# Kernel tuning notes

Measured on AMD Instinct MI355X. Metric: run time of the kernel, lower is better.

## Reference

```python
import jax, jax.numpy as jnp
import numpy as np

# --- config (mirrors the torch/keras module's config object) ---
RATIOS = np.array([0.5, 1.0, 2.0], dtype=np.float32)
SCALE = 128.0
POS_THRESH = 0.15
NMS_THRESH = 0.7
STRIDE = 16.0
H = W = 64
A = len(RATIOS)           # anchors per spatial location
N = H * W * A             # total anchors = 12288


def _conv(x, w, b):
    # NHWC input, HWIO kernel, SAME padding, stride 1
    y = jax.lax.conv_general_dilated(x, w, (1, 1), 'SAME',
                                     dimension_numbers=('NHWC', 'HWIO', 'NHWC'))
    return y + b


def _grid_anchors():
    ws = SCALE * np.sqrt(RATIOS)
    hs = SCALE / np.sqrt(RATIOS)
    base = np.stack([-ws / 2, -hs / 2, ws / 2, hs / 2], axis=1)      # [A,4]
    xs = (np.arange(W, dtype=np.float32) + 0.5) * STRIDE
    ys = (np.arange(H, dtype=np.float32) + 0.5) * STRIDE
    cx, cy = np.meshgrid(xs, ys)                                     # [H,W]
    shifts = np.stack([cx, cy, cx, cy], axis=-1).reshape(-1, 1, 4)   # [H*W,1,4]
    return jnp.asarray((shifts + base[None]).reshape(-1, 4).astype(np.float32))  # [N,4]


def _decode(anchors, deltas):
    # standard RPN box decode: (dx,dy,dw,dh) applied to (x1,y1,x2,y2) anchors
    w = anchors[:, 2] - anchors[:, 0]
    h = anchors[:, 3] - anchors[:, 1]
    xc = (anchors[:, 0] + anchors[:, 2]) * 0.5 + deltas[:, 0] * w
    yc = (anchors[:, 1] + anchors[:, 3]) * 0.5 + deltas[:, 1] * h
    nw = w * jnp.exp(deltas[:, 2])
    nh = h * jnp.exp(deltas[:, 3])
    return jnp.stack([xc - nw / 2, yc - nh / 2, xc + nw / 2, yc + nh / 2], axis=1)  # [N,4]


def _nms(boxes, keep0, thresh):
    # greedy NMS in index order (original passes scores=ones to tf NMS, so
    # the sort by score is a no-op and greedy order == index order).
    boxes = jax.lax.stop_gradient(boxes)
    x1, y1, x2, y2 = boxes[:, 0], boxes[:, 1], boxes[:, 2], boxes[:, 3]
    areas = (x2 - x1) * (y2 - y1)
    idx = jnp.arange(boxes.shape[0])

    def body(i, keep):
        xx1 = jnp.maximum(x1[i], x1)
        yy1 = jnp.maximum(y1[i], y1)
        xx2 = jnp.minimum(x2[i], x2)
        yy2 = jnp.minimum(y2[i], y2)
        inter = jnp.maximum(xx2 - xx1, 0.0) * jnp.maximum(yy2 - yy1, 0.0)
        iou = inter / (areas[i] + areas - inter + 1e-9)
        suppress = keep[i] & keep & (iou > thresh) & (idx > i)
        return keep & ~suppress

    return jax.lax.fori_loop(0, boxes.shape[0], body, keep0)


def setup_inputs() -> dict:
    key = jax.random.key(0)
    ks = jax.random.split(key, 7)
    c_in, c_mid = 1024, 512
    inputs = jax.random.normal(ks[0], (1, H, W, c_in), dtype=jnp.float32)
    conv_w = jax.random.normal(ks[1], (3, 3, c_in, c_mid), dtype=jnp.float32) * 0.01
    conv_b = jnp.zeros((c_mid,), dtype=jnp.float32)
    cls_w = jax.random.normal(ks[2], (1, 1, c_mid, 2 * A), dtype=jnp.float32) * 0.05
    cls_b = jnp.zeros((2 * A,), dtype=jnp.float32)
    reg_w = jax.random.normal(ks[3], (1, 1, c_mid, 4 * A), dtype=jnp.float32) * 0.01
    reg_b = jnp.zeros((4 * A,), dtype=jnp.float32)
    return {"inputs": inputs, "conv_w": conv_w, "conv_b": conv_b,
            "cls_w": cls_w, "cls_b": cls_b, "reg_w": reg_w, "reg_b": reg_b}


def reference(inputs, conv_w, conv_b, cls_w, cls_b, reg_w, reg_b):
    x = jax.nn.relu(_conv(inputs, conv_w, conv_b))                  # [1,H,W,512]
    cls = jax.nn.softmax(_conv(x, cls_w, cls_b), axis=-1)           # [1,H,W,2A]
    reg = _conv(x, reg_w, reg_b)                                    # [1,H,W,4A]
    scores = cls.reshape(-1, 2)[:, 1]                               # [N] fg prob
    deltas = reg.reshape(-1, 4)                                     # [N,4]
    boxes = _decode(_grid_anchors(), deltas)                        # [N,4]
    keep0 = scores > POS_THRESH
    keep = _nms(boxes, keep0, NMS_THRESH)                           # [N] bool
    # fixed-shape proposal output: suppressed / filtered boxes zeroed out
    return boxes * keep[:, None].astype(boxes.dtype)
```

## Files before the change

### kernel.cpp

```cpp
#include <hip/hip_runtime.h>
#include <cstdint>

#define NBOX 12288
#define NWORDS 192
#define POS_THRESH 0.15f
#define NMS_THRESH 0.7f

typedef unsigned long long u64;
typedef _Float16 half8 __attribute__((ext_vector_type(8)));
typedef float floatx4 __attribute__((ext_vector_type(4)));

__global__ __launch_bounds__(256) void zero_y(float4* __restrict__ Y) {
  Y[blockIdx.x * 256 + threadIdx.x] = float4{0.f, 0.f, 0.f, 0.f};
}

__global__ __launch_bounds__(256) void prep_wt(
    const float* __restrict__ Wc, _Float16* __restrict__ WTh, _Float16* __restrict__ WTl)
{
  __shared__ float tile[64][65];
  const int b = blockIdx.x;
  const int tap = b >> 7;
  const int rem = b & 127;
  const int c0 = (rem >> 3) * 64, n0 = (rem & 7) * 64;
  const int t = threadIdx.x;
  #pragma unroll
  for (int i = 0; i < 16; ++i) {
    const int idx = i * 256 + t;
    const int c = idx >> 6, n = idx & 63;
    tile[n][c] = Wc[((size_t)(tap * 1024 + c0 + c)) * 512 + n0 + n];
  }
  __syncthreads();
  #pragma unroll
  for (int i = 0; i < 16; ++i) {
    const int idx = i * 256 + t;
    const int n = idx >> 6, c = idx & 63;
    const float v = tile[n][c];
    const _Float16 h = (_Float16)v;
    const _Float16 l = (_Float16)((v - (float)h) * 4096.0f);
    const size_t o = ((size_t)(tap * 512 + n0 + n)) * 1024 + c0 + c;
    WTh[o] = h;
    WTl[o] = l;
  }
}

#define AROW 40
#define AS_PLANE (4 * 66 * AROW)
#define BS_PLANE (128 * AROW)
#define YPLANE 2097152
__global__ __launch_bounds__(256, 2) void conv_mfma(
    const float* __restrict__ X, const _Float16* __restrict__ WTh,
    const _Float16* __restrict__ WTl, float* __restrict__ Y, int partial)
{
  __shared__ _Float16 As[2 * AS_PLANE];
  __shared__ _Float16 Bs[2 * BS_PLANE];
  const int bid = blockIdx.x;
  const int ks = bid & 3;
  const int nt = (bid >> 2) & 3;
  const int mt = bid >> 4;
  const int t = threadIdx.x;
  const int lane = t & 63, wid = t >> 6;
  const int wm = wid >> 1, wn = wid & 1;
  const int lrow = lane & 15, quad = lane >> 4;

  floatx4 accH[4][4], accL[4][4];
  #pragma unroll
  for (int i = 0; i < 4; ++i)
    #pragma unroll
    for (int j = 0; j < 4; ++j) { accH[i][j] = (floatx4)0.f; accL[i][j] = (floatx4)0.f; }

  for (int kc = 0; kc < 8; ++kc) {
    const int c0 = ks * 256 + kc * 32;
    __syncthreads();
    for (int r = t; r < 264; r += 256) {
      const int yy = r / 66;
      const int xx = r - yy * 66;
      const int yi = mt * 2 + yy - 1;
      const int xi = xx - 1;
      const int akey = (r >> 3) & 3;
      _Float16* dsth = &As[r * AROW];
      _Float16* dstl = dsth + AS_PLANE;
      if (yi >= 0 && yi < 64 && xi >= 0 && xi < 64) {
        const float4* src = (const float4*)(X + ((size_t)(yi * 64 + xi)) * 1024 + c0);
        #pragma unroll
        for (int j = 0; j < 4; ++j) {
          const float4 va = src[2 * j], vb = src[2 * j + 1];
          const float f[8] = {va.x, va.y, va.z, va.w, vb.x, vb.y, vb.z, vb.w};
          half8 hh, hl;
          #pragma unroll
          for (int e = 0; e < 8; ++e) {
            const _Float16 h = (_Float16)f[e];
            hh[e] = h;
            hl[e] = (_Float16)((f[e] - (float)h) * 4096.0f);
          }
          const int sl = (j ^ akey) * 8;
          *(half8*)&dsth[sl] = hh;
          *(half8*)&dstl[sl] = hl;
        }
      } else {
        const half8 z = (half8)(_Float16)0.f;
        #pragma unroll
        for (int j = 0; j < 4; ++j) { *(half8*)&dsth[j * 8] = z; *(half8*)&dstl[j * 8] = z; }
      }
    }
    for (int tap = 0; tap < 9; ++tap) {
      if (tap > 0) __syncthreads();
      {
        const int hl = t >> 7, n = t & 127;
        const int bkey = (n >> 3) & 3;
        const _Float16* src = (hl ? WTl : WTh) +
            ((size_t)(tap * 512 + nt * 128 + n)) * 1024 + c0;
        _Float16* dst = &Bs[hl * BS_PLANE + n * AROW];
        #pragma unroll
        for (int j = 0; j < 4; ++j)
          *(half8*)&dst[(j ^ bkey) * 8] = *(const half8*)&src[j * 8];
      }
      __syncthreads();
      const int dy = tap / 3 - 1, dx = tap - (tap / 3) * 3 - 1;
      const int yy = wm + dy + 1;
      const int xxb = dx + 1;
      half8 Ah[4], Al[4], Bh[4], Bl[4];
      #pragma unroll
      for (int fm = 0; fm < 4; ++fm) {
        const int row = yy * 66 + xxb + fm * 16 + lrow;
        const int idx = row * AROW + ((quad ^ ((row >> 3) & 3)) * 8);
        Ah[fm] = *(const half8*)&As[idx];
        Al[fm] = *(const half8*)&As[idx + AS_PLANE];
      }
      #pragma unroll
      for (int fn = 0; fn < 4; ++fn) {
        const int row = wn * 64 + fn * 16 + lrow;
        const int idx = row * AROW + ((quad ^ ((row >> 3) & 3)) * 8);
        Bh[fn] = *(const half8*)&Bs[idx];
        Bl[fn] = *(const half8*)&Bs[idx + BS_PLANE];
      }
      #pragma unroll
      for (int fm = 0; fm < 4; ++fm)
        #pragma unroll
        for (int fn = 0; fn < 4; ++fn) {
          accH[fm][fn] = __builtin_amdgcn_mfma_f32_16x16x32_f16(Ah[fm], Bh[fn], accH[fm][fn], 0, 0, 0);
          accL[fm][fn] = __builtin_amdgcn_mfma_f32_16x16x32_f16(Al[fm], Bh[fn], accL[fm][fn], 0, 0, 0);
          accL[fm][fn] = __builtin_amdgcn_mfma_f32_16x16x32_f16(Ah[fm], Bl[fn], accL[fm][fn], 0, 0, 0);
        }
    }
  }
  const int m0 = mt * 128 + wm * 64;
  const int n0 = nt * 128 + wn * 64;
  if (partial) {
    float* Yp = Y + (size_t)ks * YPLANE;
    #pragma unroll
    for (int fm = 0; fm < 4; ++fm)
      #pragma unroll
      for (int fn = 0; fn < 4; ++fn) {
        const int n = n0 + fn * 16 + lrow;
        #pragma unroll
        for (int r = 0; r < 4; ++r) {
          const int m = m0 + fm * 16 + quad * 4 + r;
          Yp[(size_t)m * 512 + n] = accH[fm][fn][r] + accL[fm][fn][r] * (1.0f / 4096.0f);
        }
      }
  } else {
    #pragma unroll
    for (int fm = 0; fm < 4; ++fm)
      #pragma unroll
      for (int fn = 0; fn < 4; ++fn) {
        const int n = n0 + fn * 16 + lrow;
        #pragma unroll
        for (int r = 0; r < 4; ++r) {
          const int m = m0 + fm * 16 + quad * 4 + r;
          atomicAdd(&Y[(size_t)m * 512 + n],
                    accH[fm][fn][r] + accL[fm][fn][r] * (1.0f / 4096.0f));
        }
      }
  }
}

__global__ __launch_bounds__(64) void heads_decode(
    const float* __restrict__ Yx, int nparts, const float* __restrict__ Bc,
    const float* __restrict__ Wcls, const float* __restrict__ bcls,
    const float* __restrict__ Wreg, const float* __restrict__ breg,
    float* __restrict__ boxes, float* __restrict__ scores, int* __restrict__ ext)
{
  __shared__ float xs[512];
  const int pos = blockIdx.x;
  const int l = threadIdx.x;
  if (l == 0 && pos < NWORDS) ext[pos] = pos;
  float4 v0 = {0.f, 0.f, 0.f, 0.f};
  float4 v1 = {0.f, 0.f, 0.f, 0.f};
  for (int p = 0; p < nparts; ++p) {
    const float* xrow = Yx + (size_t)p * YPLANE + (size_t)pos * 512;
    const float4 a = *(const float4*)&xrow[l * 8];
    const float4 b = *(const float4*)&xrow[l * 8 + 4];
    v0.x += a.x; v0.y += a.y; v0.z += a.z; v0.w += a.w;
    v1.x += b.x; v1.y += b.y; v1.z += b.z; v1.w += b.w;
  }
  const float4 b0 = *(const float4*)&Bc[l * 8];
  const float4 b1 = *(const float4*)&Bc[l * 8 + 4];
  xs[l * 8 + 0] = fmaxf(v0.x + b0.x, 0.f);
  xs[l * 8 + 1] = fmaxf(v0.y + b0.y, 0.f);
  xs[l * 8 + 2] = fmaxf(v0.z + b0.z, 0.f);
  xs[l * 8 + 3] = fmaxf(v0.w + b0.w, 0.f);
  xs[l * 8 + 4] = fmaxf(v1.x + b1.x, 0.f);
  xs[l * 8 + 5] = fmaxf(v1.y + b1.y, 0.f);
  xs[l * 8 + 6] = fmaxf(v1.z + b1.z, 0.f);
  xs[l * 8 + 7] = fmaxf(v1.w + b1.w, 0.f);
  __syncthreads();

  const float* wp;
  int oc;
  float bini;
  if (l < 6)       { wp = Wcls + l;       oc = 6;  bini = bcls[l]; }
  else if (l < 18) { wp = Wreg + (l - 6); oc = 12; bini = breg[l - 6]; }
  else             { wp = Wcls;           oc = 0;  bini = 0.f; }
  float acc = bini;
  const float* p = wp;
  #pragma unroll 4
  for (int c = 0; c < 512; ++c) { acc = fmaf(xs[c], *p, acc); p += oc; }

  const float l0 = __shfl(acc, 0), l1 = __shfl(acc, 1), l2 = __shfl(acc, 2);
  const float l3 = __shfl(acc, 3), l4 = __shfl(acc, 4), l5 = __shfl(acc, 5);
  const int a = (l < 3) ? l : 0;
  const float d0 = __shfl(acc, 6 + a * 4 + 0);
  const float d1 = __shfl(acc, 6 + a * 4 + 1);
  const float d2 = __shfl(acc, 6 + a * 4 + 2);
  const float d3 = __shfl(acc, 6 + a * 4 + 3);

  const float mx = fmaxf(fmaxf(fmaxf(l0, l1), fmaxf(l2, l3)), fmaxf(l4, l5));
  const float e0 = expf(l0 - mx), e1 = expf(l1 - mx), e2 = expf(l2 - mx);
  const float e3 = expf(l3 - mx), e4 = expf(l4 - mx), e5 = expf(l5 - mx);
  const float den = ((((e0 + e1) + e2) + e3) + e4) + e5;
  const float esel = (a == 0) ? e1 : ((a == 1) ? e3 : e5);
  const float sc = esel / den;

  const int px = pos & 63, py = pos >> 6;
  const float cx = (px + 0.5f) * 16.0f;
  const float cy = (py + 0.5f) * 16.0f;
  const float ratio = (a == 0) ? 0.5f : ((a == 1) ? 1.0f : 2.0f);
  const float sq = sqrtf(ratio);
  const float wsz = 128.0f * sq;
  const float hsz = 128.0f / sq;
  const float a0 = cx - wsz * 0.5f;
  const float a1 = cy - hsz * 0.5f;
  const float a2 = cx + wsz * 0.5f;
  const float a3 = cy + hsz * 0.5f;
  const float w = a2 - a0, h = a3 - a1;
  const float xc = __fadd_rn(__fmul_rn(__fadd_rn(a0, a2), 0.5f), __fmul_rn(d0, w));
  const float yc = __fadd_rn(__fmul_rn(__fadd_rn(a1, a3), 0.5f), __fmul_rn(d1, h));
  const float nw = __fmul_rn(w, expf(d2));
  const float nh = __fmul_rn(h, expf(d3));
  float4 box;
  box.x = __fsub_rn(xc, __fmul_rn(nw, 0.5f));
  box.y = __fsub_rn(yc, __fmul_rn(nh, 0.5f));
  box.z = __fadd_rn(xc, __fmul_rn(nw, 0.5f));
  box.w = __fadd_rn(yc, __fmul_rn(nh, 0.5f));

  if (l < 3) {
    const int idx = pos * 3 + a;
    *(float4*)&boxes[idx * 4] = box;
    scores[idx] = sc;
  }
}

__global__ __launch_bounds__(256) void build_mask(
    const float* __restrict__ boxes, u64* __restrict__ maskT,
    int* __restrict__ ext)
{
  const int w  = blockIdx.x;
  const int ci = blockIdx.y;
  if (w < ci) return;
  __shared__ float4 rb[64];
  __shared__ int anyf;
  const int t = threadIdx.x;
  const int lane = t & 63, wid = t >> 6;
  if (t == 0) anyf = 0;
  if (t < 64) rb[t] = *(const float4*)&boxes[(ci * 64 + t) * 4];
  const float4 cb = *(const float4*)&boxes[(w * 64 + lane) * 4];
  const float careaa = __fmul_rn(cb.z - cb.x, cb.w - cb.y);
  const int jglob = w * 64 + lane;
  __syncthreads();
  bool any = false;
  for (int rr = 0; rr < 16; ++rr) {
    const int r = wid * 16 + rr;
    const int row = ci * 64 + r;
    const float4 rx = rb[r];
    const float ra = __fmul_rn(rx.z - rx.x, rx.w - rx.y);
    const float xx1 = fmaxf(rx.x, cb.x);
    const float yy1 = fmaxf(rx.y, cb.y);
    const float xx2 = fminf(rx.z, cb.z);
    const float yy2 = fminf(rx.w, cb.w);
    const float iw = fmaxf(__fsub_rn(xx2, xx1), 0.f);
    const float ih = fmaxf(__fsub_rn(yy2, yy1), 0.f);
    const float inter = __fmul_rn(iw, ih);
    const float den = __fadd_rn(__fsub_rn(__fadd_rn(ra, careaa), inter), 1e-9f);
    const float iou = __fdiv_rn(inter, den);
    const bool bit = (iou > NMS_THRESH) && (jglob > row);
    any |= bit;
    const u64 word = __ballot(bit ? 1 : 0);
    if (lane == 0) maskT[(size_t)w * NBOX + row] = word;
  }
  if (any) anyf = 1;
  __syncthreads();
  if (t == 0 && anyf && w > ci) atomicMax(&ext[ci], w);
}

__device__ __forceinline__ u64 rl64(unsigned lo, unsigned hi, int l) {
  const unsigned a = (unsigned)__builtin_amdgcn_readlane((int)lo, l);
  const unsigned b = (unsigned)__builtin_amdgcn_readlane((int)hi, l);
  return ((u64)b << 32) | (u64)a;
}
__device__ __forceinline__ u64 rl64v(u64 v, int ln) {
  const unsigned a = (unsigned)__builtin_amdgcn_readlane((int)(unsigned)v, ln);
  const unsigned b = (unsigned)__builtin_amdgcn_readlane((int)(unsigned)(v >> 32), ln);
  return ((u64)b << 32) | (u64)a;
}
__device__ __forceinline__ u64 shflxor64(u64 v, int m) {
  const int lo = __shfl_xor((int)(unsigned)v, m);
  const int hi = __shfl_xor((int)(unsigned)(v >> 32), m);
  return ((u64)(unsigned)hi << 32) | (unsigned)lo;
}
__device__ __forceinline__ u64 build_alive(const float* sp) {
  u64 w = 0ull;
  const float4* p = (const float4*)sp;
  #pragma unroll
  for (int q = 0; q < 16; ++q) {
    const float4 s = p[q];
    if (s.x > POS_THRESH) w |= (1ull << (q * 4 + 0));
    if (s.y > POS_THRESH) w |= (1ull << (q * 4 + 1));
    if (s.z > POS_THRESH) w |= (1ull << (q * 4 + 2));
    if (s.w > POS_THRESH) w |= (1ull << (q * 4 + 3));
  }
  return w;
}

#define NSTEPF(C_, MU, DU, MP, DP)                                              \
  do {                                                                          \
    if (t < 256) {                                                              \
      const int c_ = (C_);                                                      \
      const int e_ = extS[c_];                                                  \
      const u64 aw0v_ = alvS[c_];                                               \
      if (c_ + 1 < NWORDS) {                                                    \
        DP = maskT[(size_t)(c_ + 1) * NBOX + (size_t)(c_ + 1) * 64 + lane];     \
        const int en_ = extS[c_ + 1];                                           \
        const int t0n_ = c_ + 2 + wsub;                                         \
        if (t0n_ <= en_) {                                                      \
          const u64* cbp_ = maskT + (size_t)t0n_ * NBOX + (size_t)(c_ + 1) * 64 + sub * 8; \
          MP##0 = cbp_[0]; MP##1 = cbp_[1]; MP##2 = cbp_[2]; MP##3 = cbp_[3];   \
          MP##4 = cbp_[4]; MP##5 = cbp_[5]; MP##6 = cbp_[6]; MP##7 = cbp_[7];   \
        }                                                                       \
      }                                                                         \
      const unsigned awlo_ = (unsigned)__builtin_amdgcn_readfirstlane((int)(unsigned)(aw0v_ & 0xffffffffull)); \
      const unsigned awhi_ = (unsigned)__builtin_amdgcn_readfirstlane((int)(unsigned)(aw0v_ >> 32)); \
      const u64 aw0_ = ((u64)awhi_ << 32) | (u64)awlo_;                         \
      if (aw0_) {                                                               \
        const unsigned dlo_ = (unsigned)(DU & 0xffffffffull);                   \
        const unsigned dhi_ = (unsigned)(DU >> 32);                             \
        u64 aw_ = aw0_;                                                         \
        const bool sb_ = ((aw0_ >> lane) & 1ull) && ((DU & aw0_) != 0ull);      \
        u64 pending_ = __ballot(sb_ ? 1 : 0);                                   \
        while (pending_) {                                                      \
          const u64 p0_ = pending_;                                             \
          const u64 p1_ = p0_ & (p0_ - 1);                                      \
          const u64 p2_ = p1_ & (p1_ - 1);                                      \
          const u64 p3_ = p2_ & (p2_ - 1);                                      \
          const int b0_ = __builtin_ctzll(p0_);                                 \
          const int b1_ = p1_ ? __builtin_ctzll(p1_) : 64;                      \
          const int b2_ = p2_ ? __builtin_ctzll(p2_) : 64;                      \
          const int b3_ = p3_ ? __builtin_ctzll(p3_) : 64;                      \
          const u64 r0_ = rl64(dlo_, dhi_, b0_);                                \
          const u64 r1_ = rl64(dlo_, dhi_, b1_ & 63);                           \
          const u64 r2_ = rl64(dlo_, dhi_, b2_ & 63);                           \
          const u64 r3_ = rl64(dlo_, dhi_, b3_ & 63);                           \
          u64 supp_ = r0_;                                                      \
          u64 done_ = 1ull << b0_;                                              \
          const u64 k1_ = ((b1_ < 64) & !((supp_ >> (b1_ & 63)) & 1ull)) ? ~0ull : 0ull; \
          supp_ |= r1_ & k1_;  done_ |= (1ull << (b1_ & 63)) & k1_;             \
          const u64 k2_ = ((b2_ < 64) & !((supp_ >> (b2_ & 63)) & 1ull)) ? ~0ull : 0ull; \
          supp_ |= r2_ & k2_;  done_ |= (1ull << (b2_ & 63)) & k2_;             \
          const u64 k3_ = ((b3_ < 64) & !((supp_ >> (b3_ & 63)) & 1ull)) ? ~0ull : 0ull; \
          supp_ |= r3_ & k3_;  done_ |= (1ull << (b3_ & 63)) & k3_;             \
          aw_ &= ~supp_;                                                        \
          pending_ &= ~(supp_ | done_);                                         \
        }                                                                       \
        const int t0_ = c_ + 1 + wsub;                                          \
        if (t0_ <= e_) {                                                        \
          const unsigned oct_ = (unsigned)(aw_ >> (sub * 8)) & 0xffu;           \
          u64 sup_ = 0ull;                                                      \
          if (oct_ & 1u)   sup_ |= MU##0;                                       \
          if (oct_ & 2u)   sup_ |= MU##1;                                       \
          if (oct_ & 4u)   sup_ |= MU##2;                                       \
          if (oct_ & 8u)   sup_ |= MU##3;                                       \
          if (oct_ & 16u)  sup_ |= MU##4;                                       \
          if (oct_ & 32u)  sup_ |= MU##5;                                       \
          if (oct_ & 64u)  sup_ |= MU##6;                                       \
          if (oct_ & 128u) sup_ |= MU##7;                                       \
          if (sup_) atomicAnd((unsigned long long*)&alvS[t0_], ~sup_);          \
        }                                                                       \
        for (int base_ = c_ + 33; base_ <= e_; base_ += 32) {                   \
          const int tw_ = base_ + wsub;                                         \
          if (tw_ <= e_) {                                                      \
            const u64* cbp_ = maskT + (size_t)tw_ * NBOX + (size_t)c_ * 64 + sub * 8; \
            u64 m_[8];                                                          \
            _Pragma("unroll")                                                   \
            for (int j_ = 0; j_ < 8; ++j_) m_[j_] = cbp_[j_];                   \
            const unsigned oct_ = (unsigned)(aw_ >> (sub * 8)) & 0xffu;         \
            u64 sup_ = 0ull;                                                    \
            _Pragma("unroll")                                                   \
            for (int j_ = 0; j_ < 8; ++j_) if ((oct_ >> j_) & 1u) sup_ |= m_[j_]; \
            if (sup_) atomicAnd((unsigned long long*)&alvS[tw_], ~sup_);        \
          }                                                                     \
        }                                                                       \
        if (t == 0) alvS[c_] = aw_;                                             \
      }                                                                         \
    }                                                                           \
    asm volatile("s_waitcnt lgkmcnt(0)" ::: "memory");                          \
    __builtin_amdgcn_s_barrier();                                               \
    asm volatile("" ::: "memory");                                              \
  } while (0)

__global__ __launch_bounds__(1024) void nms_scan(
    const float* __restrict__ scores, const u64* __restrict__ maskT,
    const int* __restrict__ ext, u64* __restrict__ aliveOut)
{
  __shared__ u64 alvA[NWORDS], alvB[NWORDS], keep0S[NWORDS];
  __shared__ int extS[NWORDS], srcLoS[NWORDS];
  __shared__ int changedS;
  const int t = threadIdx.x;
  const int lane = t & 63;
  const int wv = t >> 6;
  const int g = lane >> 3;
  const int s = lane & 7;
  const int wsub = t >> 3;
  const int sub = t & 7;

  if (t < NWORDS) {
    const u64 wb = build_alive(scores + (size_t)t * 64);
    keep0S[t] = wb;
    alvA[t] = wb;
    extS[t] = ext[t];
  }
  if (t == 0) changedS = 0;
  __syncthreads();
  if (t < NWORDS) {
    int lo = t;
    for (int c = 0; c < t; ++c) if (extS[c] >= t) { lo = c; break; }
    srcLoS[t] = lo;
  }
  __syncthreads();

  int cur = 0, converged = 0;
  for (int it = 0; it < 64; ++it) {
    const u64* aOld = cur ? alvB : alvA;
    u64* aNew = cur ? alvA : alvB;
    for (int k = 0; k < 12; ++k) {
      const int w = wv + k * 16;
      const u64 dg = maskT[(size_t)w * NBOX + (size_t)w * 64 + lane];
      const int lo = srcLoS[w];
      u64 supx = 0ull;
      for (int base = lo; base < w; base += 8) {
        const int c = base + g;
        u64 part = 0ull;
        if (c < w) {
          const u64 av = aOld[c];
          const unsigned oct = (unsigned)((av >> (s * 8)) & 0xffull);
          const u64* col = maskT + (size_t)w * NBOX + (size_t)c * 64 + s * 8;
          const u64 m0 = col[0], m1 = col[1], m2 = col[2], m3 = col[3];
          const u64 m4 = col[4], m5 = col[5], m6 = col[6], m7 = col[7];
          if (oct & 1u)   part |= m0;
          if (oct & 2u)   part |= m1;
          if (oct & 4u)   part |= m2;
          if (oct & 8u)   part |= m3;
          if (oct & 16u)  part |= m4;
          if (oct & 32u)  part |= m5;
          if (oct & 64u)  part |= m6;
          if (oct & 128u) part |= m7;
        }
        part |= shflxor64(part, 1);
        part |= shflxor64(part, 2);
        part |= shflxor64(part, 4);
        part |= shflxor64(part, 8);
        part |= shflxor64(part, 16);
        part |= shflxor64(part, 32);
        supx |= part;
      }
      const u64 b0v = keep0S[w] & ~supx;
      u64 aw = b0v;
      const bool sbv = ((b0v >> lane) & 1ull) && ((dg & b0v) != 0ull);
      u64 pending = __ballot(sbv ? 1 : 0);
      while (pending) {
        const u64 q0 = pending;
        const u64 q1 = q0 & (q0 - 1);
        const u64 q2 = q1 & (q1 - 1);
        const u64 q3 = q2 & (q2 - 1);
        const int c0 = __builtin_ctzll(q0);
        const int c1 = q1 ? __builtin_ctzll(q1) : 64;
        const int c2 = q2 ? __builtin_ctzll(q2) : 64;
        const int c3 = q3 ? __builtin_ctzll(q3) : 64;
        const u64 u0 = rl64v(dg, c0);
        const u64 u1 = rl64v(dg, c1 & 63);
        const u64 u2 = rl64v(dg, c2 & 63);
        const u64 u3 = rl64v(dg, c3 & 63);
        u64 sp = u0;
        u64 dn = 1ull << c0;
        const u64 g1 = ((c1 < 64) && !((sp >> (c1 & 63)) & 1ull)) ? ~0ull : 0ull;
        sp |= u1 & g1; dn |= (1ull << (c1 & 63)) & g1;
        const u64 g2 = ((c2 < 64) && !((sp >> (c2 & 63)) & 1ull)) ? ~0ull : 0ull;
        sp |= u2 & g2; dn |= (1ull << (c2 & 63)) & g2;
        const u64 g3 = ((c3 < 64) && !((sp >> (c3 & 63)) & 1ull)) ? ~0ull : 0ull;
        sp |= u3 & g3; dn |= (1ull << (c3 & 63)) & g3;
        aw &= ~sp;
        pending &= ~(sp | dn);
      }
      if (lane == 0) {
        aNew[w] = aw;
        if (aw != aOld[w]) changedS = 1;
      }
    }
    __syncthreads();
    const int ch = changedS;
    __syncthreads();
    cur ^= 1;
    if (!ch) { converged = 1; break; }
    if (t == 0) changedS = 0;
    __syncthreads();
  }

  if (converged) {
    const u64* fin = cur ? alvB : alvA;
    if (t < NWORDS) aliveOut[t] = fin[t];
    return;
  }

  u64* alvS = alvA;
  if (t < NWORDS) alvS[t] = keep0S[t];
  __syncthreads();

  u64 mA0 = 0, mA1 = 0, mA2 = 0, mA3 = 0, mA4 = 0, mA5 = 0, mA6 = 0, mA7 = 0;
  u64 mB0 = 0, mB1 = 0, mB2 = 0, mB3 = 0, mB4 = 0, mB5 = 0, mB6 = 0, mB7 = 0;
  u64 dgA = 0, dgB = 0;
  if (t < 256) {
    const int e0f = extS[0];
    if (1 + wsub <= e0f) {
      const u64* cbp = maskT + (size_t)(1 + wsub) * NBOX + sub * 8;
      mA0 = cbp[0]; mA1 = cbp[1]; mA2 = cbp[2]; mA3 = cbp[3];
      mA4 = cbp[4]; mA5 = cbp[5]; mA6 = cbp[6]; mA7 = cbp[7];
    }
    dgA = maskT[lane];
  }
  asm volatile("s_waitcnt lgkmcnt(0)" ::: "memory");
  __builtin_amdgcn_s_barrier();
  asm volatile("" ::: "memory");

  for (int c = 0; c < NWORDS; c += 2) {
    NSTEPF(c,     mA, dgA, mB, dgB);
    NSTEPF(c + 1, mB, dgB, mA, dgA);
  }
  if (t < NWORDS) aliveOut[t] = alvS[t];
}

__global__ __launch_bounds__(256) void write_output(
    const float* __restrict__ boxes, const u64* __restrict__ alive,
    float* __restrict__ out)
{
  const int i = blockIdx.x * 256 + threadIdx.x;
  if (i < NBOX) {
    const bool k = (alive[i >> 6] >> (i & 63)) & 1ull;
    const float4 b = *(const float4*)&boxes[i * 4];
    const float4 z = {0.f, 0.f, 0.f, 0.f};
    *(float4*)&out[i * 4] = k ? b : z;
  }
}

extern "C" void kernel_launch(void* const* d_in, const int* in_sizes, int n_in,
                              void* d_out, int out_size, void* d_ws, size_t ws_size,
                              hipStream_t stream) {
  const float* X    = (const float*)d_in[0];
  const float* Wc   = (const float*)d_in[1];
  const float* Bc   = (const float*)d_in[2];
  const float* Wcls = (const float*)d_in[3];
  const float* bcls = (const float*)d_in[4];
  const float* Wreg = (const float*)d_in[5];
  const float* breg = (const float*)d_in[6];

  char* ws = (char*)d_ws;
  const size_t NEED_BIG = 52676864ull;

  if (ws_size >= NEED_BIG) {
    float*     Y4     = (float*)    (ws);
    float*     boxes  = (float*)    (ws + 33554432);
    float*     scores = (float*)    (ws + 33751040);
    u64*       aliveG = (u64*)      (ws + 33800192);
    int*       extG   = (int*)      (ws + 33801728);
    _Float16*  WTh    = (_Float16*) (ws + 33802496);
    _Float16*  WTl    = (_Float16*) (ws + 43239680);
    u64*       maskT  = (u64*)      (ws + 33802496);

    prep_wt     <<<1152, 256, 0, stream>>>(Wc, WTh, WTl);
    conv_mfma   <<<512, 256, 0, stream>>>(X, WTh, WTl, Y4, 1);
    heads_decode<<<4096, 64, 0, stream>>>(Y4, 4, Bc, Wcls, bcls, Wreg, breg, boxes, scores, extG);
    build_mask  <<<dim3(192, 192), 256, 0, stream>>>(boxes, maskT, extG);
    nms_scan    <<<1, 1024, 0, stream>>>(scores, maskT, extG, aliveG);
    write_output<<<48, 256, 0, stream>>>(boxes, aliveG, (float*)d_out);
  } else {
    float*     Y      = (float*)    (ws);
    float*     boxes  = (float*)    (ws + 8388608);
    float*     scores = (float*)    (ws + 8585216);
    u64*       aliveG = (u64*)      (ws + 8634368);
    int*       extG   = (int*)      (ws + 8635904);
    _Float16*  WTh    = (_Float16*) (ws + 8636672);
    _Float16*  WTl    = (_Float16*) (ws + 18073856);
    u64*       maskT  = (u64*)      (ws + 8636672);

    zero_y      <<<2048, 256, 0, stream>>>((float4*)Y);
    prep_wt     <<<1152, 256, 0, stream>>>(Wc, WTh, WTl);
    conv_mfma   <<<512, 256, 0, stream>>>(X, WTh, WTl, Y, 0);
    heads_decode<<<4096, 64, 0, stream>>>(Y, 1, Bc, Wcls, bcls, Wreg, breg, boxes, scores, extG);
    build_mask  <<<dim3(192, 192), 256, 0, stream>>>(boxes, maskT, extG);
    nms_scan    <<<1, 1024, 0, stream>>>(scores, maskT, extG, aliveG);
    write_output<<<48, 256, 0, stream>>>(boxes, aliveG, (float*)d_out);
  }
}
```

Before: 490.5 us.

## Use in-place Gauss-Seidel NMS iteration with contiguous word ownership and cached diagonals

The Jacobi-style fixed-point NMS iteration with double-buffered alive bitmasks becomes an in-place Gauss-Seidel update on a single shared array. Each wave now owns a contiguous block of 12 words and processes them in order, so later words immediately see suppression updates from earlier ones, which should cut the number of outer iterations needed to converge. The diagonal mask blocks are preloaded into registers once instead of being re-read every iteration. This adds register pressure and relies on monotonic convergence of in-place updates; the contiguous ownership may also unbalance work across waves.

Measured after the change: 436.5 us, median of 2. -11.0%, faster.

```diff
diff --git a/kernel.cpp b/kernel.cpp
--- a/kernel.cpp
+++ b/kernel.cpp
@@ -420,7 +420,7 @@
     const float* __restrict__ scores, const u64* __restrict__ maskT,
     const int* __restrict__ ext, u64* __restrict__ aliveOut)
 {
-  __shared__ u64 alvA[NWORDS], alvB[NWORDS], keep0S[NWORDS];
+  __shared__ u64 alvS[NWORDS], keep0S[NWORDS];
   __shared__ int extS[NWORDS], srcLoS[NWORDS];
   __shared__ int changedS;
   const int t = threadIdx.x;
@@ -434,7 +434,7 @@
   if (t < NWORDS) {
     const u64 wb = build_alive(scores + (size_t)t * 64);
     keep0S[t] = wb;
-    alvA[t] = wb;
+    alvS[t] = wb;
     extS[t] = ext[t];
   }
   if (t == 0) changedS = 0;
@@ -446,20 +446,26 @@
   }
   __syncthreads();
 
-  int cur = 0, converged = 0;
+  u64 dgR[12];
+  #pragma unroll
+  for (int k = 0; k < 12; ++k) {
+    const int w = wv * 12 + k;
+    dgR[k] = maskT[(size_t)w * NBOX + (size_t)w * 64 + lane];
+  }
+
+  int converged = 0;
   for (int it = 0; it < 64; ++it) {
-    const u64* aOld = cur ? alvB : alvA;
-    u64* aNew = cur ? alvA : alvB;
+    #pragma unroll
     for (int k = 0; k < 12; ++k) {
-      const int w = wv + k * 16;
-      const u64 dg = maskT[(size_t)w * NBOX + (size_t)w * 64 + lane];
+      const int w = wv * 12 + k;
       const int lo = srcLoS[w];
+      const u64 dg = dgR[k];
       u64 supx = 0ull;
       for (int base = lo; base < w; base += 8) {
         const int c = base + g;
         u64 part = 0ull;
         if (c < w) {
-          const u64 av = aOld[c];
+          const u64 av = alvS[c];
           const unsigned oct = (unsigned)((av >> (s * 8)) & 0xffull);
           const u64* col = maskT + (size_t)w * NBOX + (size_t)c * 64 + s * 8;
           const u64 m0 = col[0], m1 = col[1], m2 = col[2], m3 = col[3];
@@ -510,26 +516,23 @@
         pending &= ~(sp | dn);
       }
       if (lane == 0) {
-        aNew[w] = aw;
-        if (aw != aOld[w]) changedS = 1;
-      }
+        if (aw != alvS[w]) { alvS[w] = aw; changedS = 1; }
+      }
+      asm volatile("s_waitcnt lgkmcnt(0)" ::: "memory");
     }
     __syncthreads();
     const int ch = changedS;
     __syncthreads();
-    cur ^= 1;
     if (!ch) { converged = 1; break; }
     if (t == 0) changedS = 0;
     __syncthreads();
   }
 
   if (converged) {
-    const u64* fin = cur ? alvB : alvA;
-    if (t < NWORDS) aliveOut[t] = fin[t];
+    if (t < NWORDS) aliveOut[t] = alvS[t];
     return;
   }
 
-  u64* alvS = alvA;
   if (t < NWORDS) alvS[t] = keep0S[t];
   __syncthreads();
 
```
